# Optimization experiments

Hardware: AMD Instinct MI355X
Metric: run time of the kernel (lower is better)

Reference implementation:

```python
import jax, jax.numpy as jnp
import numpy as np

IN_F = 4096
OUT_F = 4096
BATCH = 8192


def setup_inputs() -> dict:
    key = jax.random.key(0)
    ks = jax.random.split(key, 7)
    bound = 1.0 / np.sqrt(IN_F)
    return {
        "x": jax.random.normal(ks[0], (BATCH, IN_F), dtype=jnp.float32),
        "weight_mu": jax.random.normal(ks[1], (OUT_F, IN_F), dtype=jnp.float32) * np.sqrt(2.0 / IN_F),  # kaiming fan_in relu
        "weight_log_var": jnp.full((OUT_F, IN_F), -6.0, dtype=jnp.float32),
        "bias_mu": jax.random.uniform(ks[2], (OUT_F,), dtype=jnp.float32, minval=-bound, maxval=bound),
        "bias_log_var": jnp.full((OUT_F,), -6.0, dtype=jnp.float32),
        "weight_eps": jax.random.normal(ks[3], (OUT_F, IN_F), dtype=jnp.float32),
        "bias_eps": jax.random.normal(ks[4], (OUT_F,), dtype=jnp.float32),
    }


def reference(x, weight_mu, weight_log_var, bias_mu, bias_log_var, weight_eps, bias_eps):
    # Reparameterized sampling: w = mu + eps * exp(0.5 * log_var)
    weight = weight_mu + weight_eps * jnp.exp(0.5 * weight_log_var)   # [out, in]
    bias = bias_mu + bias_eps * jnp.exp(0.5 * bias_log_var)           # [out]
    # F.linear(x, weight, bias) = x @ weight.T + bias
    return jnp.einsum("bi,oi->bo", x, weight) + bias
```

## Files before the change

kernel.cpp:

```cpp
#include <hip/hip_runtime.h>
#include <hip/hip_bf16.h>
#include <stdint.h>

typedef __bf16 bf16x8 __attribute__((ext_vector_type(8)));
typedef float f32x4 __attribute__((ext_vector_type(4)));
typedef unsigned short u16x8 __attribute__((ext_vector_type(8)));

__device__ inline unsigned short f2bf_rne(float f) {
  unsigned int u = __float_as_uint(f);
  u += 0x7fffu + ((u >> 16) & 1u);
  return (unsigned short)(u >> 16);
}

__global__ __launch_bounds__(256) void prep_weight(
    const float4* __restrict__ mu, const float4* __restrict__ lv,
    const float4* __restrict__ eps, u16x8* __restrict__ wbf, int n8) {
  int i = blockIdx.x * 256 + threadIdx.x;
  if (i >= n8) return;
  float4 m0 = mu[2 * i], m1 = mu[2 * i + 1];
  float4 v0 = lv[2 * i], v1 = lv[2 * i + 1];
  float4 e0 = eps[2 * i], e1 = eps[2 * i + 1];
  u16x8 p;
  p[0] = f2bf_rne(m0.x + e0.x * __expf(0.5f * v0.x));
  p[1] = f2bf_rne(m0.y + e0.y * __expf(0.5f * v0.y));
  p[2] = f2bf_rne(m0.z + e0.z * __expf(0.5f * v0.z));
  p[3] = f2bf_rne(m0.w + e0.w * __expf(0.5f * v0.w));
  p[4] = f2bf_rne(m1.x + e1.x * __expf(0.5f * v1.x));
  p[5] = f2bf_rne(m1.y + e1.y * __expf(0.5f * v1.y));
  p[6] = f2bf_rne(m1.z + e1.z * __expf(0.5f * v1.z));
  p[7] = f2bf_rne(m1.w + e1.w * __expf(0.5f * v1.w));
  wbf[i] = p;
}

__global__ __launch_bounds__(256) void prep_x(
    const float4* __restrict__ x, u16x8* __restrict__ xbf, int n8) {
  int i = blockIdx.x * 256 + threadIdx.x;
  if (i >= n8) return;
  float4 m0 = x[2 * i], m1 = x[2 * i + 1];
  u16x8 p;
  p[0] = f2bf_rne(m0.x); p[1] = f2bf_rne(m0.y);
  p[2] = f2bf_rne(m0.z); p[3] = f2bf_rne(m0.w);
  p[4] = f2bf_rne(m1.x); p[5] = f2bf_rne(m1.y);
  p[6] = f2bf_rne(m1.z); p[7] = f2bf_rne(m1.w);
  xbf[i] = p;
}

#define BM 128
#define BN 128
#define BK 64

__global__ __launch_bounds__(256) void gemm_bt_bias(
    const unsigned short* __restrict__ A,
    const unsigned short* __restrict__ B,
    const float* __restrict__ bmu, const float* __restrict__ blv,
    const float* __restrict__ beps,
    float* __restrict__ C, int M, int N, int K) {
  __shared__ __align__(16) unsigned short As[BM * BK];
  __shared__ __align__(16) unsigned short Bs[BN * BK];

  const int tid  = threadIdx.x;
  const int wave = tid >> 6;
  const int lane = tid & 63;
  const int wm = wave >> 1;
  const int wn = wave & 1;

  const int rowA0 = blockIdx.y * BM;
  const int rowB0 = blockIdx.x * BN;

  const int srow = tid >> 3;
  const int scol = (((tid & 7) ^ ((tid >> 3) & 7))) * 8;

  f32x4 acc[4][4];
#pragma unroll
  for (int i = 0; i < 4; ++i)
#pragma unroll
    for (int j = 0; j < 4; ++j)
      acc[i][j] = (f32x4){0.f, 0.f, 0.f, 0.f};

  const int mrow = lane & 15;
  const int gsel = lane >> 4;

  for (int k0 = 0; k0 < K; k0 += BK) {
#pragma unroll
    for (int j = 0; j < 4; ++j) {
      const int r = j * 32 + srow;
      const unsigned short* gA = A + (size_t)(rowA0 + r) * K + k0 + scol;
      const unsigned short* gB = B + (size_t)(rowB0 + r) * K + k0 + scol;
      __builtin_amdgcn_global_load_lds(
          (const __attribute__((address_space(1))) unsigned int*)gA,
          (__attribute__((address_space(3))) unsigned int*)&As[(j * 256 + wave * 64) * 8],
          16, 0, 0);
      __builtin_amdgcn_global_load_lds(
          (const __attribute__((address_space(1))) unsigned int*)gB,
          (__attribute__((address_space(3))) unsigned int*)&Bs[(j * 256 + wave * 64) * 8],
          16, 0, 0);
    }
    __syncthreads();

#pragma unroll
    for (int kk = 0; kk < BK; kk += 32) {
      bf16x8 af[4], bfv[4];
#pragma unroll
      for (int mi = 0; mi < 4; ++mi) {
        const int row = wm * 64 + mi * 16 + mrow;
        const int pg = ((kk >> 3) + gsel) ^ (mrow & 7);
        af[mi] = *(const bf16x8*)&As[row * BK + pg * 8];
      }
#pragma unroll
      for (int ni = 0; ni < 4; ++ni) {
        const int row = wn * 64 + ni * 16 + mrow;
        const int pg = ((kk >> 3) + gsel) ^ (mrow & 7);
        bfv[ni] = *(const bf16x8*)&Bs[row * BK + pg * 8];
      }
#pragma unroll
      for (int mi = 0; mi < 4; ++mi)
#pragma unroll
        for (int ni = 0; ni < 4; ++ni)
          acc[mi][ni] = __builtin_amdgcn_mfma_f32_16x16x32_bf16(
              af[mi], bfv[ni], acc[mi][ni], 0, 0, 0);
    }
    __syncthreads();
  }

  const int colq = lane & 15;
  const int rq4  = (lane >> 4) * 4;
#pragma unroll
  for (int ni = 0; ni < 4; ++ni) {
    const int col = rowB0 + wn * 64 + ni * 16 + colq;
    const float bias = bmu[col] + beps[col] * __expf(0.5f * blv[col]);
#pragma unroll
    for (int mi = 0; mi < 4; ++mi) {
      const int rbase = rowA0 + wm * 64 + mi * 16 + rq4;
#pragma unroll
      for (int r = 0; r < 4; ++r)
        C[(size_t)(rbase + r) * N + col] = acc[mi][ni][r] + bias;
    }
  }
}

extern "C" void kernel_launch(void* const* d_in, const int* in_sizes, int n_in,
                              void* d_out, int out_size, void* d_ws, size_t ws_size,
                              hipStream_t stream) {
  const float* x    = (const float*)d_in[0];
  const float* wmu  = (const float*)d_in[1];
  const float* wlv  = (const float*)d_in[2];
  const float* bmu  = (const float*)d_in[3];
  const float* blv  = (const float*)d_in[4];
  const float* weps = (const float*)d_in[5];
  const float* beps = (const float*)d_in[6];
  float* out = (float*)d_out;

  const int M = 8192, N = 4096, K = 4096;

  unsigned short* xbf = (unsigned short*)d_ws;
  unsigned short* wbf = xbf + (size_t)M * K;

  const int n8w = N * K / 8;
  prep_weight<<<n8w / 256, 256, 0, stream>>>(
      (const float4*)wmu, (const float4*)wlv, (const float4*)weps,
      (u16x8*)wbf, n8w);
  const int n8x = M * K / 8;
  prep_x<<<n8x / 256, 256, 0, stream>>>((const float4*)x, (u16x8*)xbf, n8x);

  dim3 grid(N / BN, M / BM);
  gemm_bt_bias<<<grid, 256, 0, stream>>>(xbf, wbf, bmu, blv, beps, out, M, N, K);
}
```

Before: 673.2 us.

## Triple-buffer GEMM LDS tiles with async prefetch and XCD-aware block remap

Restructures the bf16 MFMA GEMM main loop so that K tiles (now BK=32) are staged into three LDS buffers two iterations ahead. It uses vmcnt waits and a single barrier per iteration instead of two __syncthreads, so global loads overlap with MFMA compute. The launch becomes a 1D grid with a block-index remap that groups neighbouring tiles per XCD to improve L2 reuse. It also adds s_setprio around the MFMA block and a 3-blocks-per-CU launch bound. The smaller BK halves the MFMA work per barrier and may add sync overhead, and the occupancy hint may constrain registers.

```diff
diff --git a/kernel.cpp b/kernel.cpp
--- a/kernel.cpp
+++ b/kernel.cpp
@@ -47,16 +47,17 @@
 
 #define BM 128
 #define BN 128
-#define BK 64
-
-__global__ __launch_bounds__(256) void gemm_bt_bias(
+#define BK 32
+#define NBUF 3
+
+__global__ __launch_bounds__(256, 3) void gemm_bt_bias(
     const unsigned short* __restrict__ A,
     const unsigned short* __restrict__ B,
     const float* __restrict__ bmu, const float* __restrict__ blv,
     const float* __restrict__ beps,
     float* __restrict__ C, int M, int N, int K) {
-  __shared__ __align__(16) unsigned short As[BM * BK];
-  __shared__ __align__(16) unsigned short Bs[BN * BK];
+  __shared__ __align__(16) unsigned short As[NBUF][BM * BK];
+  __shared__ __align__(16) unsigned short Bs[NBUF][BN * BK];
 
   const int tid  = threadIdx.x;
   const int wave = tid >> 6;
@@ -64,11 +65,42 @@
   const int wm = wave >> 1;
   const int wn = wave & 1;
 
-  const int rowA0 = blockIdx.y * BM;
-  const int rowB0 = blockIdx.x * BN;
-
-  const int srow = tid >> 3;
-  const int scol = (((tid & 7) ^ ((tid >> 3) & 7))) * 8;
+  const int cpx = gridDim.x >> 3;
+  const int bid = (blockIdx.x & 7) * cpx + (blockIdx.x >> 3);
+  const int ntx = N / BN;
+  const int by  = bid / ntx;
+  const int bx  = bid - by * ntx;
+  const int rowA0 = by * BM;
+  const int rowB0 = bx * BN;
+
+  const int srow = tid >> 2;
+  const int scol = ((tid & 3) ^ (srow & 3)) * 8;
+  const unsigned short* pA0 = A + (size_t)(rowA0 + srow) * K + scol;
+  const unsigned short* pA1 = pA0 + (size_t)64 * K;
+  const unsigned short* pB0 = B + (size_t)(rowB0 + srow) * K + scol;
+  const unsigned short* pB1 = pB0 + (size_t)64 * K;
+  const int ldsg = wave * 512;
+
+#define STAGE(kt, buf)                                                          \
+  do {                                                                          \
+    const size_t ko_ = (size_t)(kt) * BK;                                       \
+    __builtin_amdgcn_global_load_lds(                                           \
+        (const __attribute__((address_space(1))) unsigned int*)(pA0 + ko_),     \
+        (__attribute__((address_space(3))) unsigned int*)&As[buf][ldsg],        \
+        16, 0, 0);                                                              \
+    __builtin_amdgcn_global_load_lds(                                           \
+        (const __attribute__((address_space(1))) unsigned int*)(pA1 + ko_),     \
+        (__attribute__((address_space(3))) unsigned int*)&As[buf][2048 + ldsg], \
+        16, 0, 0);                                                              \
+    __builtin_amdgcn_global_load_lds(                                           \
+        (const __attribute__((address_space(1))) unsigned int*)(pB0 + ko_),     \
+        (__attribute__((address_space(3))) unsigned int*)&Bs[buf][ldsg],        \
+        16, 0, 0);                                                              \
+    __builtin_amdgcn_global_load_lds(                                           \
+        (const __attribute__((address_space(1))) unsigned int*)(pB1 + ko_),     \
+        (__attribute__((address_space(3))) unsigned int*)&Bs[buf][2048 + ldsg], \
+        16, 0, 0);                                                              \
+  } while (0)
 
   f32x4 acc[4][4];
 #pragma unroll
@@ -79,47 +111,47 @@
 
   const int mrow = lane & 15;
   const int gsel = lane >> 4;
-
-  for (int k0 = 0; k0 < K; k0 += BK) {
-#pragma unroll
-    for (int j = 0; j < 4; ++j) {
-      const int r = j * 32 + srow;
-      const unsigned short* gA = A + (size_t)(rowA0 + r) * K + k0 + scol;
-      const unsigned short* gB = B + (size_t)(rowB0 + r) * K + k0 + scol;
-      __builtin_amdgcn_global_load_lds(
-          (const __attribute__((address_space(1))) unsigned int*)gA,
-          (__attribute__((address_space(3))) unsigned int*)&As[(j * 256 + wave * 64) * 8],
-          16, 0, 0);
-      __builtin_amdgcn_global_load_lds(
-          (const __attribute__((address_space(1))) unsigned int*)gB,
-          (__attribute__((address_space(3))) unsigned int*)&Bs[(j * 256 + wave * 64) * 8],
-          16, 0, 0);
+  const int pgo  = (gsel ^ (mrow & 3)) * 8;
+  const int aoff = (wm * 64 + mrow) * BK + pgo;
+  const int boff = (wn * 64 + mrow) * BK + pgo;
+
+  STAGE(0, 0);
+  STAGE(1, 1);
+  asm volatile("s_waitcnt vmcnt(4)" ::: "memory");
+  __builtin_amdgcn_s_barrier();
+  __builtin_amdgcn_sched_barrier(0);
+
+  const int NT = K / BK;
+  int cur = 0;
+  for (int t = 0; t < NT; ++t) {
+    if (t + 2 < NT) {
+      int b2 = cur + 2; if (b2 >= NBUF) b2 -= NBUF;
+      STAGE(t + 2, b2);
     }
-    __syncthreads();
-
-#pragma unroll
-    for (int kk = 0; kk < BK; kk += 32) {
-      bf16x8 af[4], bfv[4];
-#pragma unroll
-      for (int mi = 0; mi < 4; ++mi) {
-        const int row = wm * 64 + mi * 16 + mrow;
-        const int pg = ((kk >> 3) + gsel) ^ (mrow & 7);
-        af[mi] = *(const bf16x8*)&As[row * BK + pg * 8];
-      }
-#pragma unroll
-      for (int ni = 0; ni < 4; ++ni) {
-        const int row = wn * 64 + ni * 16 + mrow;
-        const int pg = ((kk >> 3) + gsel) ^ (mrow & 7);
-        bfv[ni] = *(const bf16x8*)&Bs[row * BK + pg * 8];
-      }
-#pragma unroll
-      for (int mi = 0; mi < 4; ++mi)
-#pragma unroll
-        for (int ni = 0; ni < 4; ++ni)
-          acc[mi][ni] = __builtin_amdgcn_mfma_f32_16x16x32_bf16(
-              af[mi], bfv[ni], acc[mi][ni], 0, 0, 0);
+    const unsigned short* as = &As[cur][0];
+    const unsigned short* bs = &Bs[cur][0];
+    bf16x8 af[4], bfv[4];
+#pragma unroll
+    for (int mi = 0; mi < 4; ++mi)
+      af[mi] = *(const bf16x8*)&as[aoff + mi * (16 * BK)];
+#pragma unroll
+    for (int ni = 0; ni < 4; ++ni)
+      bfv[ni] = *(const bf16x8*)&bs[boff + ni * (16 * BK)];
+    __builtin_amdgcn_s_setprio(1);
+#pragma unroll
+    for (int mi = 0; mi < 4; ++mi)
+#pragma unroll
+      for (int ni = 0; ni < 4; ++ni)
+        acc[mi][ni] = __builtin_amdgcn_mfma_f32_16x16x32_bf16(
+            af[mi], bfv[ni], acc[mi][ni], 0, 0, 0);
+    __builtin_amdgcn_s_setprio(0);
+    if (t + 1 < NT) {
+      if (t + 2 < NT) { asm volatile("s_waitcnt vmcnt(4)" ::: "memory"); }
+      else            { asm volatile("s_waitcnt vmcnt(0)" ::: "memory"); }
+      __builtin_amdgcn_s_barrier();
+      __builtin_amdgcn_sched_barrier(0);
     }
-    __syncthreads();
+    ++cur; if (cur >= NBUF) cur = 0;
   }
 
   const int colq = lane & 15;
@@ -136,6 +168,7 @@
         C[(size_t)(rbase + r) * N + col] = acc[mi][ni][r] + bias;
     }
   }
+#undef STAGE
 }
 
 extern "C" void kernel_launch(void* const* d_in, const int* in_sizes, int n_in,
@@ -162,6 +195,6 @@
   const int n8x = M * K / 8;
   prep_x<<<n8x / 256, 256, 0, stream>>>((const float4*)x, (u16x8*)xbf, n8x);
 
-  dim3 grid(N / BN, M / BM);
+  dim3 grid((M / BM) * (N / BN));
   gemm_bt_bias<<<grid, 256, 0, stream>>>(xbf, wbf, bmu, blv, beps, out, M, N, K);
 }
```

Result: slower. 687.7 us (+2.1%).

## Triple-buffer GEMM tiles with 512-thread blocks and interleaved MFMA/load schedule

Applied to the files above, without the earlier changes.

The GEMM block tile grows to 256x128 with 8 waves. Global-to-LDS loads now run through a 3-stage ring buffer that prefetches two tiles ahead. Each K-step is split into four phases that interleave staged loads, LDS fragment reads and MFMA groups, using s_setprio, explicit vmcnt waits and barriers. The goal is to hide global and LDS latency behind matrix-core work. In exchange it uses more LDS (~144KB per block), adds more barriers per K-step, and relies on delicate hand-written waitcnt accounting.

```diff
diff --git a/kernel.cpp b/kernel.cpp
--- a/kernel.cpp
+++ b/kernel.cpp
@@ -45,18 +45,19 @@
   xbf[i] = p;
 }
 
-#define BM 128
+#define BM 256
 #define BN 128
 #define BK 64
-
-__global__ __launch_bounds__(256) void gemm_bt_bias(
+#define NBUF 3
+
+__global__ __launch_bounds__(512, 2) void gemm_bt_bias(
     const unsigned short* __restrict__ A,
     const unsigned short* __restrict__ B,
     const float* __restrict__ bmu, const float* __restrict__ blv,
     const float* __restrict__ beps,
     float* __restrict__ C, int M, int N, int K) {
-  __shared__ __align__(16) unsigned short As[BM * BK];
-  __shared__ __align__(16) unsigned short Bs[BN * BK];
+  __shared__ __align__(16) unsigned short As[NBUF][BM * BK];
+  __shared__ __align__(16) unsigned short Bs[NBUF][BN * BK];
 
   const int tid  = threadIdx.x;
   const int wave = tid >> 6;
@@ -68,7 +69,29 @@
   const int rowB0 = blockIdx.x * BN;
 
   const int srow = tid >> 3;
-  const int scol = (((tid & 7) ^ ((tid >> 3) & 7))) * 8;
+  const int scol = ((tid & 7) ^ (srow & 7)) * 8;
+  const unsigned short* gA0 = A + (size_t)(rowA0 + srow) * K + scol;
+  const unsigned short* gA1 = gA0 + (size_t)64 * K;
+  const unsigned short* gA2 = gA0 + (size_t)128 * K;
+  const unsigned short* gA3 = gA0 + (size_t)192 * K;
+  const unsigned short* gB0 = B + (size_t)(rowB0 + srow) * K + scol;
+  const unsigned short* gB1 = gB0 + (size_t)64 * K;
+  const int dep = wave * 512;
+
+#define GLL(srcp, dstp)                                                     \
+  __builtin_amdgcn_global_load_lds(                                         \
+      (const __attribute__((address_space(1))) unsigned int*)(srcp),        \
+      (__attribute__((address_space(3))) unsigned int*)(dstp), 16, 0, 0)
+
+#define STAGE_A01(kt, b) do { const size_t ko_ = (size_t)(kt) * BK;          \
+    GLL(gA0 + ko_, &As[b][dep]);                                             \
+    GLL(gA1 + ko_, &As[b][4096 + dep]); } while (0)
+#define STAGE_A23(kt, b) do { const size_t ko_ = (size_t)(kt) * BK;          \
+    GLL(gA2 + ko_, &As[b][8192 + dep]);                                      \
+    GLL(gA3 + ko_, &As[b][12288 + dep]); } while (0)
+#define STAGE_B01(kt, b) do { const size_t ko_ = (size_t)(kt) * BK;          \
+    GLL(gB0 + ko_, &Bs[b][dep]);                                             \
+    GLL(gB1 + ko_, &Bs[b][4096 + dep]); } while (0)
 
   f32x4 acc[4][4];
 #pragma unroll
@@ -79,47 +102,101 @@
 
   const int mrow = lane & 15;
   const int gsel = lane >> 4;
-
-  for (int k0 = 0; k0 < K; k0 += BK) {
-#pragma unroll
-    for (int j = 0; j < 4; ++j) {
-      const int r = j * 32 + srow;
-      const unsigned short* gA = A + (size_t)(rowA0 + r) * K + k0 + scol;
-      const unsigned short* gB = B + (size_t)(rowB0 + r) * K + k0 + scol;
-      __builtin_amdgcn_global_load_lds(
-          (const __attribute__((address_space(1))) unsigned int*)gA,
-          (__attribute__((address_space(3))) unsigned int*)&As[(j * 256 + wave * 64) * 8],
-          16, 0, 0);
-      __builtin_amdgcn_global_load_lds(
-          (const __attribute__((address_space(1))) unsigned int*)gB,
-          (__attribute__((address_space(3))) unsigned int*)&Bs[(j * 256 + wave * 64) * 8],
-          16, 0, 0);
-    }
-    __syncthreads();
-
-#pragma unroll
-    for (int kk = 0; kk < BK; kk += 32) {
-      bf16x8 af[4], bfv[4];
-#pragma unroll
-      for (int mi = 0; mi < 4; ++mi) {
-        const int row = wm * 64 + mi * 16 + mrow;
-        const int pg = ((kk >> 3) + gsel) ^ (mrow & 7);
-        af[mi] = *(const bf16x8*)&As[row * BK + pg * 8];
-      }
-#pragma unroll
-      for (int ni = 0; ni < 4; ++ni) {
-        const int row = wn * 64 + ni * 16 + mrow;
-        const int pg = ((kk >> 3) + gsel) ^ (mrow & 7);
-        bfv[ni] = *(const bf16x8*)&Bs[row * BK + pg * 8];
-      }
-#pragma unroll
-      for (int mi = 0; mi < 4; ++mi)
-#pragma unroll
-        for (int ni = 0; ni < 4; ++ni)
-          acc[mi][ni] = __builtin_amdgcn_mfma_f32_16x16x32_bf16(
-              af[mi], bfv[ni], acc[mi][ni], 0, 0, 0);
-    }
-    __syncthreads();
+  const int pg0  = ((0 + gsel) ^ (mrow & 7)) * 8;
+  const int pg32 = ((4 + gsel) ^ (mrow & 7)) * 8;
+  const int abase = (wm * 64 + mrow) * BK;
+  const int bbase = (wn * 64 + mrow) * BK;
+
+#define RD_A(mi, pg, bufp) (*(const bf16x8*)&(bufp)[abase + (mi)*1024 + (pg)])
+#define RD_B(ni, pg, bufp) (*(const bf16x8*)&(bufp)[bbase + (ni)*1024 + (pg)])
+
+  STAGE_A01(0, 0); STAGE_A23(0, 0); STAGE_B01(0, 0);
+  STAGE_A01(1, 1); STAGE_A23(1, 1); STAGE_B01(1, 1);
+  asm volatile("s_waitcnt vmcnt(6)" ::: "memory");
+  __builtin_amdgcn_s_barrier();
+  __builtin_amdgcn_sched_barrier(0);
+
+  bf16x8 bL[4], bH[4], a0, a1, a2, a3, t0, t1;
+  {
+    const unsigned short* as0 = &As[0][0];
+    const unsigned short* bs0 = &Bs[0][0];
+#pragma unroll
+    for (int ni = 0; ni < 4; ++ni) bL[ni] = RD_B(ni, pg0, bs0);
+    a0 = RD_A(0, pg0, as0);
+    a1 = RD_A(1, pg0, as0);
+  }
+
+  const int NT = K / BK;
+  int c = 0;
+  for (int t = 0; t < NT; ++t) {
+    const int n = (c + 1 < NBUF) ? c + 1 : 0;
+    const int w = (c + 2 < NBUF) ? c + 2 : c + 2 - NBUF;
+    const unsigned short* asc = &As[c][0];
+    const unsigned short* bsc = &Bs[c][0];
+    const bool pf = (t + 2 < NT);
+
+    if (pf) STAGE_A01(t + 2, w);
+    a2 = RD_A(2, pg0, asc);
+    a3 = RD_A(3, pg0, asc);
+    __builtin_amdgcn_s_setprio(1);
+#pragma unroll
+    for (int ni = 0; ni < 4; ++ni) {
+      acc[0][ni] = __builtin_amdgcn_mfma_f32_16x16x32_bf16(a0, bL[ni], acc[0][ni], 0, 0, 0);
+      acc[1][ni] = __builtin_amdgcn_mfma_f32_16x16x32_bf16(a1, bL[ni], acc[1][ni], 0, 0, 0);
+    }
+    __builtin_amdgcn_s_setprio(0);
+    __builtin_amdgcn_s_barrier();
+    __builtin_amdgcn_sched_barrier(0);
+
+    if (pf) STAGE_A23(t + 2, w);
+#pragma unroll
+    for (int ni = 0; ni < 4; ++ni) bH[ni] = RD_B(ni, pg32, bsc);
+    t0 = RD_A(0, pg32, asc);
+    t1 = RD_A(1, pg32, asc);
+    __builtin_amdgcn_s_setprio(1);
+#pragma unroll
+    for (int ni = 0; ni < 4; ++ni) {
+      acc[2][ni] = __builtin_amdgcn_mfma_f32_16x16x32_bf16(a2, bL[ni], acc[2][ni], 0, 0, 0);
+      acc[3][ni] = __builtin_amdgcn_mfma_f32_16x16x32_bf16(a3, bL[ni], acc[3][ni], 0, 0, 0);
+    }
+    __builtin_amdgcn_s_setprio(0);
+    __builtin_amdgcn_s_barrier();
+    __builtin_amdgcn_sched_barrier(0);
+
+    if (pf) STAGE_B01(t + 2, w);
+    a2 = RD_A(2, pg32, asc);
+    a3 = RD_A(3, pg32, asc);
+    __builtin_amdgcn_s_setprio(1);
+#pragma unroll
+    for (int ni = 0; ni < 4; ++ni) {
+      acc[0][ni] = __builtin_amdgcn_mfma_f32_16x16x32_bf16(t0, bH[ni], acc[0][ni], 0, 0, 0);
+      acc[1][ni] = __builtin_amdgcn_mfma_f32_16x16x32_bf16(t1, bH[ni], acc[1][ni], 0, 0, 0);
+    }
+    __builtin_amdgcn_s_setprio(0);
+    if (pf) { asm volatile("s_waitcnt vmcnt(6)" ::: "memory"); }
+    else    { asm volatile("s_waitcnt vmcnt(0)" ::: "memory"); }
+    __builtin_amdgcn_s_barrier();
+    __builtin_amdgcn_sched_barrier(0);
+
+    if (t + 1 < NT) {
+      const unsigned short* asn = &As[n][0];
+      const unsigned short* bsn = &Bs[n][0];
+#pragma unroll
+      for (int ni = 0; ni < 4; ++ni) bL[ni] = RD_B(ni, pg0, bsn);
+      a0 = RD_A(0, pg0, asn);
+      a1 = RD_A(1, pg0, asn);
+    }
+    __builtin_amdgcn_s_setprio(1);
+#pragma unroll
+    for (int ni = 0; ni < 4; ++ni) {
+      acc[2][ni] = __builtin_amdgcn_mfma_f32_16x16x32_bf16(a2, bH[ni], acc[2][ni], 0, 0, 0);
+      acc[3][ni] = __builtin_amdgcn_mfma_f32_16x16x32_bf16(a3, bH[ni], acc[3][ni], 0, 0, 0);
+    }
+    __builtin_amdgcn_s_setprio(0);
+    __builtin_amdgcn_s_barrier();
+    __builtin_amdgcn_sched_barrier(0);
+
+    c = n;
   }
 
   const int colq = lane & 15;
@@ -136,6 +213,12 @@
         C[(size_t)(rbase + r) * N + col] = acc[mi][ni][r] + bias;
     }
   }
+#undef GLL
+#undef STAGE_A01
+#undef STAGE_A23
+#undef STAGE_B01
+#undef RD_A
+#undef RD_B
 }
 
 extern "C" void kernel_launch(void* const* d_in, const int* in_sizes, int n_in,
@@ -163,5 +246,5 @@
   prep_x<<<n8x / 256, 256, 0, stream>>>((const float4*)x, (u16x8*)xbf, n8x);
 
   dim3 grid(N / BN, M / BM);
-  gemm_bt_bias<<<grid, 256, 0, stream>>>(xbf, wbf, bmu, blv, beps, out, M, N, K);
-}
+  gemm_bt_bias<<<grid, 512, 0, stream>>>(xbf, wbf, bmu, blv, beps, out, M, N, K);
+}
```

After: 746.2 us. 1.11x slower.

## Use 256x256 tiles with 8 waves and double-buffered LDS prefetch pipeline

Applied to the files above, without the earlier changes.

Enlarges the GEMM block tile to 256x256 with 512 threads and splits LDS into two buffers so global-to-LDS loads for tile t+2 run while computing tile t. The MFMA work is split into four quadrant phases, each with interleaved LDS fragment loads, barriers and s_setprio, to overlap memory with matrix math. This raises data reuse per byte loaded and hides load latency, at the cost of 128KB LDS per block, which allows only one block per CU, plus heavy register use.

```diff
diff --git a/kernel.cpp b/kernel.cpp
--- a/kernel.cpp
+++ b/kernel.cpp
@@ -45,81 +45,161 @@
   xbf[i] = p;
 }
 
-#define BM 128
-#define BN 128
-#define BK 64
-
-__global__ __launch_bounds__(256) void gemm_bt_bias(
+__global__ __launch_bounds__(512, 2) void gemm_bt_bias(
     const unsigned short* __restrict__ A,
     const unsigned short* __restrict__ B,
     const float* __restrict__ bmu, const float* __restrict__ blv,
     const float* __restrict__ beps,
     float* __restrict__ C, int M, int N, int K) {
-  __shared__ __align__(16) unsigned short As[BM * BK];
-  __shared__ __align__(16) unsigned short Bs[BN * BK];
+  __shared__ __align__(16) unsigned short As[2][2][128 * 64];
+  __shared__ __align__(16) unsigned short Bs[2][2][128 * 64];
 
   const int tid  = threadIdx.x;
   const int wave = tid >> 6;
   const int lane = tid & 63;
-  const int wm = wave >> 1;
-  const int wn = wave & 1;
-
-  const int rowA0 = blockIdx.y * BM;
-  const int rowB0 = blockIdx.x * BN;
+  const int wm = wave >> 2;
+  const int wn = wave & 3;
+
+  const int rowA0 = blockIdx.y * 256;
+  const int rowB0 = blockIdx.x * 256;
 
   const int srow = tid >> 3;
-  const int scol = (((tid & 7) ^ ((tid >> 3) & 7))) * 8;
-
-  f32x4 acc[4][4];
-#pragma unroll
-  for (int i = 0; i < 4; ++i)
+  const int scol = ((tid & 7) ^ (srow & 7)) * 8;
+  const unsigned short* pA = A + (size_t)(rowA0 + srow) * K + scol;
+  const unsigned short* pB = B + (size_t)(rowB0 + srow) * K + scol;
+  const int dep = wave * 512;
+
+#define GLL(srcp, dstp)                                                     \
+  __builtin_amdgcn_global_load_lds(                                         \
+      (const __attribute__((address_space(1))) unsigned int*)(srcp),        \
+      (__attribute__((address_space(3))) unsigned int*)(dstp), 16, 0, 0)
+
+#define STAGE_A(kt, b, h) do {                                              \
+    const unsigned short* s_ = pA + (size_t)((h) * 128) * K + (size_t)(kt) * 64; \
+    GLL(s_, &As[b][h][dep]);                                                \
+    GLL(s_ + (size_t)64 * K, &As[b][h][4096 + dep]); } while (0)
+#define STAGE_B(kt, b, h) do {                                              \
+    const unsigned short* s_ = pB + (size_t)((h) * 128) * K + (size_t)(kt) * 64; \
+    GLL(s_, &Bs[b][h][dep]);                                                \
+    GLL(s_ + (size_t)64 * K, &Bs[b][h][4096 + dep]); } while (0)
+
+  f32x4 acc[8][4];
+#pragma unroll
+  for (int i = 0; i < 8; ++i)
 #pragma unroll
     for (int j = 0; j < 4; ++j)
       acc[i][j] = (f32x4){0.f, 0.f, 0.f, 0.f};
 
   const int mrow = lane & 15;
   const int gsel = lane >> 4;
-
-  for (int k0 = 0; k0 < K; k0 += BK) {
-#pragma unroll
-    for (int j = 0; j < 4; ++j) {
-      const int r = j * 32 + srow;
-      const unsigned short* gA = A + (size_t)(rowA0 + r) * K + k0 + scol;
-      const unsigned short* gB = B + (size_t)(rowB0 + r) * K + k0 + scol;
-      __builtin_amdgcn_global_load_lds(
-          (const __attribute__((address_space(1))) unsigned int*)gA,
-          (__attribute__((address_space(3))) unsigned int*)&As[(j * 256 + wave * 64) * 8],
-          16, 0, 0);
-      __builtin_amdgcn_global_load_lds(
-          (const __attribute__((address_space(1))) unsigned int*)gB,
-          (__attribute__((address_space(3))) unsigned int*)&Bs[(j * 256 + wave * 64) * 8],
-          16, 0, 0);
-    }
-    __syncthreads();
-
-#pragma unroll
-    for (int kk = 0; kk < BK; kk += 32) {
-      bf16x8 af[4], bfv[4];
-#pragma unroll
-      for (int mi = 0; mi < 4; ++mi) {
-        const int row = wm * 64 + mi * 16 + mrow;
-        const int pg = ((kk >> 3) + gsel) ^ (mrow & 7);
-        af[mi] = *(const bf16x8*)&As[row * BK + pg * 8];
-      }
-#pragma unroll
-      for (int ni = 0; ni < 4; ++ni) {
-        const int row = wn * 64 + ni * 16 + mrow;
-        const int pg = ((kk >> 3) + gsel) ^ (mrow & 7);
-        bfv[ni] = *(const bf16x8*)&Bs[row * BK + pg * 8];
-      }
-#pragma unroll
-      for (int mi = 0; mi < 4; ++mi)
-#pragma unroll
-        for (int ni = 0; ni < 4; ++ni)
+  const int pgL = (gsel ^ (mrow & 7)) * 8;
+  const int pgH = ((4 + gsel) ^ (mrow & 7)) * 8;
+  const int aoff = mrow * 64;
+  const int boff = ((wn & 1) * 64 + mrow) * 64;
+
+  STAGE_A(0, 0, 0); STAGE_A(0, 0, 1); STAGE_B(0, 0, 0); STAGE_B(0, 0, 1);
+  STAGE_A(1, 1, 0); STAGE_A(1, 1, 1); STAGE_B(1, 1, 0); STAGE_B(1, 1, 1);
+  asm volatile("s_waitcnt vmcnt(8)" ::: "memory");
+  __builtin_amdgcn_s_barrier();
+  __builtin_amdgcn_sched_barrier(0);
+
+  bf16x8 a0[4][2], a1[4][2], b01[2][2], b23[2][2];
+
+  const int NT = K / 64;
+  for (int t = 0; t < NT; ++t) {
+    const int c = t & 1;
+    const unsigned short* as = &As[c][wm][0];
+    const unsigned short* bs = &Bs[c][wn >> 1][0];
+    const bool pf = (t + 2 < NT);
+
+#pragma unroll
+    for (int mi = 0; mi < 4; ++mi) {
+      a0[mi][0] = *(const bf16x8*)&as[aoff + mi * 1024 + pgL];
+      a0[mi][1] = *(const bf16x8*)&as[aoff + mi * 1024 + pgH];
+    }
+#pragma unroll
+    for (int ni = 0; ni < 2; ++ni) {
+      b01[ni][0] = *(const bf16x8*)&bs[boff + ni * 1024 + pgL];
+      b01[ni][1] = *(const bf16x8*)&bs[boff + ni * 1024 + pgH];
+    }
+    __builtin_amdgcn_s_barrier();
+    asm volatile("s_waitcnt lgkmcnt(0)" ::: "memory");
+    __builtin_amdgcn_sched_barrier(0);
+    __builtin_amdgcn_s_setprio(1);
+#pragma unroll
+    for (int kk = 0; kk < 2; ++kk)
+#pragma unroll
+      for (int mi = 0; mi < 4; ++mi)
+#pragma unroll
+        for (int ni = 0; ni < 2; ++ni)
           acc[mi][ni] = __builtin_amdgcn_mfma_f32_16x16x32_bf16(
-              af[mi], bfv[ni], acc[mi][ni], 0, 0, 0);
-    }
-    __syncthreads();
+              a0[mi][kk], b01[ni][kk], acc[mi][ni], 0, 0, 0);
+    __builtin_amdgcn_s_setprio(0);
+    __builtin_amdgcn_s_barrier();
+    __builtin_amdgcn_sched_barrier(0);
+
+#pragma unroll
+    for (int mi = 0; mi < 4; ++mi) {
+      a1[mi][0] = *(const bf16x8*)&as[aoff + (mi + 4) * 1024 + pgL];
+      a1[mi][1] = *(const bf16x8*)&as[aoff + (mi + 4) * 1024 + pgH];
+    }
+    __builtin_amdgcn_s_barrier();
+    asm volatile("s_waitcnt lgkmcnt(0)" ::: "memory");
+    __builtin_amdgcn_sched_barrier(0);
+    __builtin_amdgcn_s_setprio(1);
+#pragma unroll
+    for (int kk = 0; kk < 2; ++kk)
+#pragma unroll
+      for (int mi = 0; mi < 4; ++mi)
+#pragma unroll
+        for (int ni = 0; ni < 2; ++ni)
+          acc[mi + 4][ni] = __builtin_amdgcn_mfma_f32_16x16x32_bf16(
+              a1[mi][kk], b01[ni][kk], acc[mi + 4][ni], 0, 0, 0);
+    __builtin_amdgcn_s_setprio(0);
+    __builtin_amdgcn_s_barrier();
+    __builtin_amdgcn_sched_barrier(0);
+
+#pragma unroll
+    for (int ni = 0; ni < 2; ++ni) {
+      b23[ni][0] = *(const bf16x8*)&bs[boff + (ni + 2) * 1024 + pgL];
+      b23[ni][1] = *(const bf16x8*)&bs[boff + (ni + 2) * 1024 + pgH];
+    }
+    if (pf) { STAGE_A(t + 2, c, 0); STAGE_A(t + 2, c, 1); }
+    __builtin_amdgcn_s_barrier();
+    asm volatile("s_waitcnt lgkmcnt(0)" ::: "memory");
+    __builtin_amdgcn_sched_barrier(0);
+    __builtin_amdgcn_s_setprio(1);
+#pragma unroll
+    for (int kk = 0; kk < 2; ++kk)
+#pragma unroll
+      for (int mi = 0; mi < 4; ++mi)
+#pragma unroll
+        for (int ni = 0; ni < 2; ++ni)
+          acc[mi + 4][ni + 2] = __builtin_amdgcn_mfma_f32_16x16x32_bf16(
+              a1[mi][kk], b23[ni][kk], acc[mi + 4][ni + 2], 0, 0, 0);
+    __builtin_amdgcn_s_setprio(0);
+    __builtin_amdgcn_s_barrier();
+    __builtin_amdgcn_sched_barrier(0);
+
+    if (pf) { STAGE_B(t + 2, c, 0); STAGE_B(t + 2, c, 1); }
+    __builtin_amdgcn_s_barrier();
+    __builtin_amdgcn_sched_barrier(0);
+    __builtin_amdgcn_s_setprio(1);
+#pragma unroll
+    for (int kk = 0; kk < 2; ++kk)
+#pragma unroll
+      for (int mi = 0; mi < 4; ++mi)
+#pragma unroll
+        for (int ni = 0; ni < 2; ++ni)
+          acc[mi][ni + 2] = __builtin_amdgcn_mfma_f32_16x16x32_bf16(
+              a0[mi][kk], b23[ni][kk], acc[mi][ni + 2], 0, 0, 0);
+    __builtin_amdgcn_s_setprio(0);
+    if (t + 1 < NT) {
+      if (pf) { asm volatile("s_waitcnt vmcnt(8)" ::: "memory"); }
+      else    { asm volatile("s_waitcnt vmcnt(0)" ::: "memory"); }
+    }
+    __builtin_amdgcn_s_barrier();
+    __builtin_amdgcn_sched_barrier(0);
   }
 
   const int colq = lane & 15;
@@ -129,13 +209,16 @@
     const int col = rowB0 + wn * 64 + ni * 16 + colq;
     const float bias = bmu[col] + beps[col] * __expf(0.5f * blv[col]);
 #pragma unroll
-    for (int mi = 0; mi < 4; ++mi) {
-      const int rbase = rowA0 + wm * 64 + mi * 16 + rq4;
+    for (int mi = 0; mi < 8; ++mi) {
+      const int rbase = rowA0 + wm * 128 + mi * 16 + rq4;
 #pragma unroll
       for (int r = 0; r < 4; ++r)
         C[(size_t)(rbase + r) * N + col] = acc[mi][ni][r] + bias;
     }
   }
+#undef GLL
+#undef STAGE_A
+#undef STAGE_B
 }
 
 extern "C" void kernel_launch(void* const* d_in, const int* in_sizes, int n_in,
@@ -162,6 +245,6 @@
   const int n8x = M * K / 8;
   prep_x<<<n8x / 256, 256, 0, stream>>>((const float4*)x, (u16x8*)xbf, n8x);
 
-  dim3 grid(N / BN, M / BM);
-  gemm_bt_bias<<<grid, 256, 0, stream>>>(xbf, wbf, bmu, blv, beps, out, M, N, K);
-}
+  dim3 grid(N / 256, M / 256);
+  gemm_bt_bias<<<grid, 512, 0, stream>>>(xbf, wbf, bmu, blv, beps, out, M, N, K);
+}
```

New measurement: 631.7 us. -6.2%, faster.
